# Performance work log

Hardware: AMD Instinct MI355X
Metric: run time of the kernel (lower is better)

## Reference

```python
import jax, jax.numpy as jnp
import numpy as np

H = 16  # num_heads
T, B, E = 1024, 4, 1024


def _gauss(mu, rho, eps):
    # Bayesian weight sample: sigma = log1p(exp(rho)) = softplus(rho)
    return mu + jax.nn.softplus(rho) * eps


def _rel_shift(x):
    # Transformer-XL relative shift. x: [B, H, Q, K]
    b, h, q, k = x.shape
    x = jnp.pad(x, ((0, 0), (0, 0), (0, 0), (1, 0)))  # zero col at front of K
    x = x.reshape(b, h, k + 1, q)
    return x[:, :, 1:, :].reshape(b, h, q, k)


def setup_inputs() -> dict:
    key = jax.random.key(0)
    ks = iter(jax.random.split(key, 32))
    std = float(np.sqrt(2.0 / (E + E)))

    def nrm(shape, s=std):
        return jax.random.normal(next(ks), shape, dtype=jnp.float32) * s

    def rho(shape):
        return jax.random.uniform(next(ks), shape, dtype=jnp.float32, minval=-5.0, maxval=-4.0)

    inp = {
        'x': jax.random.normal(next(ks), (T, B, E), dtype=jnp.float32),
        'pos': jax.random.normal(next(ks), (T, 1, E), dtype=jnp.float32),
        'attn_mask': jnp.triu(jnp.ones((T, T), dtype=bool), k=1),  # True = masked future
        'in_w_mu': nrm((3 * E, E)), 'in_w_rho': rho((3 * E, E)), 'in_w_eps': nrm((3 * E, E), 1.0),
        'in_b_mu': jnp.zeros((3 * E,), jnp.float32), 'in_b_rho': rho((3 * E,)), 'in_b_eps': nrm((3 * E,), 1.0),
        'pos_w_mu': nrm((E, E)), 'pos_w_rho': rho((E, E)), 'pos_w_eps': nrm((E, E), 1.0),
        'pos_b_mu': jnp.zeros((E,), jnp.float32), 'pos_b_rho': rho((E,)), 'pos_b_eps': nrm((E,), 1.0),
        'out_w_mu': nrm((E, E)), 'out_w_rho': rho((E, E)), 'out_w_eps': nrm((E, E), 1.0),
        'out_b_mu': jnp.zeros((E,), jnp.float32), 'out_b_rho': rho((E,)), 'out_b_eps': nrm((E,), 1.0),
        'rw_mu': nrm((H, E // H)), 'rw_rho': rho((H, E // H)), 'rw_eps': nrm((H, E // H), 1.0),
        'rr_mu': nrm((H, E // H)), 'rr_rho': rho((H, E // H)), 'rr_eps': nrm((H, E // H), 1.0),
    }
    return inp


def reference(x, pos, attn_mask,
              in_w_mu, in_w_rho, in_w_eps, in_b_mu, in_b_rho, in_b_eps,
              pos_w_mu, pos_w_rho, pos_w_eps, pos_b_mu, pos_b_rho, pos_b_eps,
              out_w_mu, out_w_rho, out_w_eps, out_b_mu, out_b_rho, out_b_eps,
              rw_mu, rw_rho, rw_eps, rr_mu, rr_rho, rr_eps):
    t, b, e = x.shape
    d = e // H

    in_w = _gauss(in_w_mu, in_w_rho, in_w_eps)
    in_b = _gauss(in_b_mu, in_b_rho, in_b_eps)
    pos_w = _gauss(pos_w_mu, pos_w_rho, pos_w_eps)
    pos_b = _gauss(pos_b_mu, pos_b_rho, pos_b_eps)
    out_w = _gauss(out_w_mu, out_w_rho, out_w_eps)
    out_b = _gauss(out_b_mu, out_b_rho, out_b_eps)
    r_w_bias = _gauss(rw_mu, rw_rho, rw_eps)  # [H, d]
    r_r_bias = _gauss(rr_mu, rr_rho, rr_eps)  # [H, d]

    qkv = x @ in_w.T + in_b                       # [T, B, 3E]
    q, k, v = jnp.split(qkv, 3, axis=-1)
    q = q.reshape(t, b, H, d)
    k = k.reshape(t, b, H, d)
    v = v.reshape(t, b, H, d)

    r = (pos[:, 0, :] @ pos_w.T + pos_b).reshape(-1, H, d)  # [R, H, d], R == klen

    scale = 1.0 / jnp.sqrt(jnp.asarray(d, x.dtype))
    AC = jnp.einsum('ibhd,jbhd->bhij', q + r_w_bias, k)            # content score
    BD = _rel_shift(jnp.einsum('ibhd,jhd->bhij', q + r_r_bias, r))  # position score
    scores = (AC + BD) * scale                                      # [B, H, T, T]

    neg = jnp.asarray(-1e9, scores.dtype)
    scores = jnp.where(attn_mask[None, None], neg, scores)

    probs = jax.nn.softmax(scores, axis=-1)
    ctx = jnp.einsum('bhij,jbhd->ibhd', probs, v).reshape(t, b, e)
    out = ctx @ out_w.T + out_b                   # [T, B, E]
    return out
```

## Files before the change

kernel.cpp:

```cpp
#include <hip/hip_runtime.h>

typedef unsigned short ushort_t;
typedef __attribute__((ext_vector_type(8))) short short8;
typedef __attribute__((ext_vector_type(4))) float f32x4;
typedef __attribute__((ext_vector_type(4))) unsigned short ush4;

#define MFMA_BF16(a, b, c) __builtin_amdgcn_mfma_f32_16x16x32_bf16((a), (b), (c), 0, 0, 0)

#define GLOAD_LDS16(GP, LP)                                                       \
  __builtin_amdgcn_global_load_lds(                                               \
      (const __attribute__((address_space(1))) void*)(GP),                        \
      (__attribute__((address_space(3))) void*)(LP), 16, 0, 0)

#define T_LEN 1024
#define BATCH 4
#define NHEAD 16
#define DHEAD 64
#define EMB 1024

__device__ __forceinline__ ushort_t f2bf(float f) {
  unsigned u = __float_as_uint(f);
  u += 0x7fffu + ((u >> 16) & 1u);
  return (ushort_t)(u >> 16);
}

__global__ void sample_w_kernel(const float* __restrict__ im, const float* __restrict__ ir,
                                const float* __restrict__ ie, ushort_t* __restrict__ io,
                                const float* __restrict__ pm, const float* __restrict__ pr,
                                const float* __restrict__ pe, ushort_t* __restrict__ po,
                                const float* __restrict__ om, const float* __restrict__ orh,
                                const float* __restrict__ oe, ushort_t* __restrict__ oo) {
  int i = blockIdx.x * 256 + threadIdx.x;
  const float *mu, *rho, *eps;
  ushort_t* out;
  int j;
  if (i < 786432) { mu = im; rho = ir; eps = ie; out = io; j = i; }
  else if (i < 1048576) { mu = pm; rho = pr; eps = pe; out = po; j = i - 786432; }
  else { mu = om; rho = orh; eps = oe; out = oo; j = i - 1048576; }
  f32x4 m = *(const f32x4*)(mu + (size_t)j * 4);
  f32x4 r = *(const f32x4*)(rho + (size_t)j * 4);
  f32x4 e = *(const f32x4*)(eps + (size_t)j * 4);
  ush4 o;
#pragma unroll
  for (int k = 0; k < 4; ++k) o[k] = f2bf(m[k] + log1pf(__expf(r[k])) * e[k]);
  *(ush4*)(out + (size_t)j * 4) = o;
}

__global__ void sample_bias_kernel(
    const float* __restrict__ am, const float* __restrict__ ar, const float* __restrict__ ae, float* __restrict__ ao,
    const float* __restrict__ bm, const float* __restrict__ br, const float* __restrict__ be, float* __restrict__ bo,
    const float* __restrict__ cm, const float* __restrict__ cr, const float* __restrict__ ce, float* __restrict__ co,
    const float* __restrict__ dm, const float* __restrict__ dr, const float* __restrict__ de, float* __restrict__ dof,
    const float* __restrict__ em, const float* __restrict__ er, const float* __restrict__ ee, float* __restrict__ eo) {
  int i = blockIdx.x * 256 + threadIdx.x;
  if (i < 3072) {
    ao[i] = am[i] + log1pf(__expf(ar[i])) * ae[i];
  } else if (i < 4096) {
    int j = i - 3072; bo[j] = bm[j] + log1pf(__expf(br[j])) * be[j];
  } else if (i < 5120) {
    int j = i - 4096; co[j] = cm[j] + log1pf(__expf(cr[j])) * ce[j];
  } else if (i < 6144) {
    int j = i - 5120; dof[j] = dm[j] + log1pf(__expf(dr[j])) * de[j];
  } else if (i < 7168) {
    int j = i - 6144; eo[j] = em[j] + log1pf(__expf(er[j])) * ee[j];
  }
}

__global__ void cast_bf16x4_kernel(const float* __restrict__ in, ushort_t* __restrict__ out, int n4) {
  int i = blockIdx.x * 256 + threadIdx.x;
  if (i < n4) {
    f32x4 v = *(const f32x4*)(in + (size_t)i * 4);
    ush4 o;
#pragma unroll
    for (int j = 0; j < 4; ++j) o[j] = f2bf(v[j]);
    *(ush4*)(out + (size_t)i * 4) = o;
  }
}

__global__ void zero_rhp_pad_kernel(ushort_t* __restrict__ rhp) {
  int idx = blockIdx.x * 256 + threadIdx.x;
  int dd = idx & 63;
  int pr = (idx >> 6) & 127;
  int h = idx >> 13;
  int phys = (pr < 64) ? pr : (pr - 64 + 1088);
  rhp[((size_t)h * 1152 + phys) * 64 + dd] = 0;
}

__global__ __launch_bounds__(256, 2)
void gemm_bt_kernel(const ushort_t* __restrict__ A, const ushort_t* __restrict__ Bt,
                    const float* __restrict__ bias, float* __restrict__ C,
                    int M, int N, int K) {
  __shared__ ushort_t As[128 * 32];
  __shared__ ushort_t Bs[128 * 32];
  const int tid = threadIdx.x;
  const int w = tid >> 6, l = tid & 63;
  const int m0 = blockIdx.x * 128, n0 = blockIdx.y * 128;
  const int wr = w >> 1, wc = w & 1;
  const int fr = l & 15, fk = (l >> 4) * 8;

  f32x4 acc[4][4] = {};

  for (int k0 = 0; k0 < K; k0 += 32) {
    __syncthreads();
#pragma unroll
    for (int p = 0; p < 2; ++p) {
      int c = p * 256 + tid;
      int row = c >> 2, col = (c & 3) * 8;
      GLOAD_LDS16(&A[(size_t)(m0 + row) * K + k0 + col], &As[c * 8]);
      GLOAD_LDS16(&Bt[(size_t)(n0 + row) * K + k0 + col], &Bs[c * 8]);
    }
    __syncthreads();
    short8 af[4], bf[4];
#pragma unroll
    for (int mi = 0; mi < 4; ++mi) af[mi] = *(const short8*)(&As[(wr * 64 + mi * 16 + fr) * 32 + fk]);
#pragma unroll
    for (int ni = 0; ni < 4; ++ni) bf[ni] = *(const short8*)(&Bs[(wc * 64 + ni * 16 + fr) * 32 + fk]);
#pragma unroll
    for (int mi = 0; mi < 4; ++mi)
#pragma unroll
      for (int ni = 0; ni < 4; ++ni)
        acc[mi][ni] = MFMA_BF16(af[mi], bf[ni], acc[mi][ni]);
  }

#pragma unroll
  for (int ni = 0; ni < 4; ++ni) {
    int col = n0 + wc * 64 + ni * 16 + fr;
    float bv = bias[col];
#pragma unroll
    for (int mi = 0; mi < 4; ++mi) {
#pragma unroll
      for (int q = 0; q < 4; ++q) {
        int row = m0 + wr * 64 + mi * 16 + (l >> 4) * 4 + q;
        C[(size_t)row * N + col] = acc[mi][ni][q] + bv;
      }
    }
  }
}

__global__ __launch_bounds__(256, 2)
void gemm_qkvpos_kernel(const ushort_t* __restrict__ x_bf, const ushort_t* __restrict__ in_w_bf,
                        const float* __restrict__ in_b,
                        const float* __restrict__ rwb, const float* __restrict__ rrb,
                        const ushort_t* __restrict__ posx_bf, const ushort_t* __restrict__ pos_w_bf,
                        const float* __restrict__ pos_b,
                        ushort_t* __restrict__ qrw, ushort_t* __restrict__ qrr,
                        ushort_t* __restrict__ kbuf, ushort_t* __restrict__ vt,
                        ushort_t* __restrict__ rhp) {
  __shared__ ushort_t As[128 * 32];
  __shared__ ushort_t Bs[128 * 32];
  const int K = 1024;
  const int tid = threadIdx.x;
  const int w = tid >> 6, l = tid & 63;
  const int bid = blockIdx.x;
  const bool isPos = bid >= 768;
  int m0, n0;
  const ushort_t *A, *Bt;
  if (!isPos) {
    m0 = (bid & 31) * 128; n0 = (bid >> 5) * 128; A = x_bf; Bt = in_w_bf;
  } else {
    int pb2 = bid - 768;
    m0 = (pb2 & 7) * 128; n0 = (pb2 >> 3) * 128; A = posx_bf; Bt = pos_w_bf;
  }
  const int wr = w >> 1, wc = w & 1;
  const int fr = l & 15, fk = (l >> 4) * 8;

  f32x4 acc[4][4] = {};

  for (int k0 = 0; k0 < K; k0 += 32) {
    __syncthreads();
#pragma unroll
    for (int p = 0; p < 2; ++p) {
      int c = p * 256 + tid;
      int row = c >> 2, col = (c & 3) * 8;
      GLOAD_LDS16(&A[(size_t)(m0 + row) * K + k0 + col], &As[c * 8]);
      GLOAD_LDS16(&Bt[(size_t)(n0 + row) * K + k0 + col], &Bs[c * 8]);
    }
    __syncthreads();
    short8 af[4], bf[4];
#pragma unroll
    for (int mi = 0; mi < 4; ++mi) af[mi] = *(const short8*)(&As[(wr * 64 + mi * 16 + fr) * 32 + fk]);
#pragma unroll
    for (int ni = 0; ni < 4; ++ni) bf[ni] = *(const short8*)(&Bs[(wc * 64 + ni * 16 + fr) * 32 + fk]);
#pragma unroll
    for (int mi = 0; mi < 4; ++mi)
#pragma unroll
      for (int ni = 0; ni < 4; ++ni)
        acc[mi][ni] = MFMA_BF16(af[mi], bf[ni], acc[mi][ni]);
  }

  if (!isPos) {
#pragma unroll
    for (int ni = 0; ni < 4; ++ni) {
      int col = n0 + wc * 64 + ni * 16 + fr;
      int part = col >> 10;
      int e = col & 1023;
      int hh = e >> 6, dd = e & 63;
      float bv = in_b[col];
      float rwv = rwb[e];
      float rrv = rrb[e];
#pragma unroll
      for (int mi = 0; mi < 4; ++mi) {
#pragma unroll
        for (int q = 0; q < 4; ++q) {
          int row = m0 + wr * 64 + mi * 16 + (l >> 4) * 4 + q;
          int t = row >> 2, b = row & 3;
          float v = acc[mi][ni][q] + bv;
          if (part == 0) {
            unsigned idx = (((unsigned)(b * 16 + hh) * 1024 + t) << 6) + dd;
            qrw[idx] = f2bf(v + rwv);
            qrr[idx] = f2bf(v + rrv);
          } else if (part == 1) {
            unsigned idx = (((unsigned)(b * 16 + hh) * 1024 + t) << 6) + dd;
            kbuf[idx] = f2bf(v);
          } else {
            vt[(((unsigned)(b * 16 + hh) * 64 + dd) << 10) + t] = f2bf(v);
          }
        }
      }
    }
  } else {
#pragma unroll
    for (int ni = 0; ni < 4; ++ni) {
      int col = n0 + wc * 64 + ni * 16 + fr;
      int hh = col >> 6, dd = col & 63;
      float bv = pos_b[col];
#pragma unroll
      for (int mi = 0; mi < 4; ++mi) {
#pragma unroll
        for (int q = 0; q < 4; ++q) {
          int t = m0 + wr * 64 + mi * 16 + (l >> 4) * 4 + q;
          rhp[((unsigned)hh * 1152 + 64 + t) * 64 + dd] = f2bf(acc[mi][ni][q] + bv);
        }
      }
    }
  }
}

__global__ __launch_bounds__(256, 2)
void attn_kernel(const ushort_t* __restrict__ qrw, const ushort_t* __restrict__ qrr,
                 const ushort_t* __restrict__ kb, const ushort_t* __restrict__ vt,
                 const ushort_t* __restrict__ rhp, ushort_t* __restrict__ ctx) {
  __shared__ __attribute__((aligned(16))) ushort_t KV[2][8192];
  __shared__ __attribute__((aligned(16))) char PtB[4][2048];

  const int tid = threadIdx.x, w = tid >> 6, l = tid & 63;
  const int bid = blockIdx.x;
  const int g = bid & 63;
  const int h = ((g & 7) << 1) | ((g >> 3) & 1);
  const int b = g >> 4;
  const int bh = b * 16 + h;
  const int p = bid >> 6;
  const int istA = (15 - p) * 64 + w * 16;
  const int istB = p * 64 + w * 16;
  const int njt = 16 - p;
  const int njtB = p + 1;
  const int fr = l & 15, fkq = (l >> 4) * 8;
  const float scale = 0.125f;
  char* Pw = PtB[w];

  short8 aqwA0, aqwA1, aqrA0, aqrA1, aqwB0, aqwB1, aqrB0, aqrB1;
  {
    unsigned qa = ((unsigned)bh * T_LEN + istA + fr) * 64 + fkq;
    aqwA0 = *(const short8*)(qrw + qa);
    aqwA1 = *(const short8*)(qrw + qa + 32);
    aqrA0 = *(const short8*)(qrr + qa);
    aqrA1 = *(const short8*)(qrr + qa + 32);
    unsigned qb = ((unsigned)bh * T_LEN + istB + fr) * 64 + fkq;
    aqwB0 = *(const short8*)(qrw + qb);
    aqwB1 = *(const short8*)(qrw + qb + 32);
    aqrB0 = *(const short8*)(qrr + qb);
    aqrB1 = *(const short8*)(qrr + qb + 32);
  }

  const int srow = 16 * w + (l >> 3);
  const unsigned sswz = (unsigned)(((l & 7) ^ (l >> 3)) << 4);
  const unsigned kgcol = (unsigned)(l & 7) * 8;
  const unsigned swzr = (unsigned)(fr & 7) << 4;

  const unsigned rbaseA = ((unsigned)h * 1152 + 64 + 1008 - istA + fr) * 64 + fkq;
  const unsigned rbaseB = ((unsigned)h * 1152 + 64 + 1008 - istB + fr) * 64 + fkq;

  float sA[4] = {0.f, 0.f, 0.f, 0.f}, sB[4] = {0.f, 0.f, 0.f, 0.f};
  f32x4 oA[4] = {}, oB[4] = {};

  short8 sg0, sg1, sg2, sg3;
#define STAGE_LOAD(J0)                                                              \
  do {                                                                              \
    sg0 = *(const short8*)(kb + ((unsigned)bh * 1024 + (unsigned)(J0) + srow) * 64 + kgcol);      \
    sg1 = *(const short8*)(kb + ((unsigned)bh * 1024 + (unsigned)(J0) + srow + 8) * 64 + kgcol);  \
    sg2 = *(const short8*)(vt + ((unsigned)bh * 64 + srow) * 1024 + (unsigned)(J0) + kgcol);      \
    sg3 = *(const short8*)(vt + ((unsigned)bh * 64 + srow + 8) * 1024 + (unsigned)(J0) + kgcol);  \
  } while (0)
#define STAGE_WRITE(BUF)                                                            \
  do {                                                                              \
    char* KS_ = (char*)KV[BUF];                                                     \
    *(short8*)(KS_ + (unsigned)srow * 128 + sswz) = sg0;                            \
    *(short8*)(KS_ + (unsigned)(srow + 8) * 128 + sswz) = sg1;                      \
    *(short8*)(KS_ + 8192 + (unsigned)srow * 128 + sswz) = sg2;                     \
    *(short8*)(KS_ + 8192 + (unsigned)(srow + 8) * 128 + sswz) = sg3;               \
  } while (0)

#define STRIP_TILE(AQW0, AQW1, AQR0, AQR1, RBASE, IST, SRUN, OACC)                   \
  do {                                                                               \
    short8 rf[10];                                                                   \
    unsigned roff = (RBASE) + (unsigned)j0 * 64;                                     \
    _Pragma("unroll")                                                                \
    for (int f = 0; f < 5; ++f) {                                                    \
      rf[2 * f] = *(const short8*)(rhp + roff + f * 1024);                           \
      rf[2 * f + 1] = *(const short8*)(rhp + roff + f * 1024 + 32);                  \
    }                                                                                \
    f32x4 ac[4] = {};                                                                \
    f32x4 pb[5] = {};                                                                \
    {                                                                                \
      short8 kf[8];                                                                  \
      _Pragma("unroll")                                                              \
      for (int f = 0; f < 4; ++f) {                                                  \
        unsigned rowb = (unsigned)(f * 16 + fr) * 128;                               \
        kf[2 * f] = *(const short8*)(KS + rowb + (((unsigned)fkq * 2) ^ swzr));      \
        kf[2 * f + 1] = *(const short8*)(KS + rowb + (((unsigned)fkq * 2 + 64) ^ swzr)); \
      }                                                                              \
      __builtin_amdgcn_s_setprio(1);                                                 \
      _Pragma("unroll")                                                              \
      for (int f = 0; f < 4; ++f) {                                                  \
        ac[f] = MFMA_BF16(AQW0, kf[2 * f], ac[f]);                                   \
        ac[f] = MFMA_BF16(AQW1, kf[2 * f + 1], ac[f]);                               \
      }                                                                              \
      _Pragma("unroll")                                                              \
      for (int f = 0; f < 5; ++f) {                                                  \
        pb[f] = MFMA_BF16(AQR0, rf[2 * f], pb[f]);                                   \
        pb[f] = MFMA_BF16(AQR1, rf[2 * f + 1], pb[f]);                               \
      }                                                                              \
      __builtin_amdgcn_s_setprio(0);                                                 \
    }                                                                                \
    _Pragma("unroll")                                                                \
    for (int q = 0; q < 4; ++q) {                                                    \
      int ri = 4 * (l >> 4) + q;                                                     \
      int e = 15 + fr - ri;                                                          \
      int src = (l & 48) | (e & 15);                                                 \
      float sh[5];                                                                   \
      _Pragma("unroll")                                                              \
      for (int f = 0; f < 5; ++f) sh[f] = __shfl(pb[f][q], src, 64);                 \
      int hi = e >> 4;                                                               \
      int ig = (IST) + ri;                                                           \
      _Pragma("unroll")                                                              \
      for (int ni = 0; ni < 4; ++ni) {                                               \
        float pv = hi ? sh[ni + 1] : sh[ni];                                         \
        float s = (ac[ni][q] + pv) * scale - 20.0f;                                  \
        int jg = j0 + ni * 16 + fr;                                                  \
        float pp = (jg > ig) ? 0.f : __expf(s);                                      \
        *(ushort_t*)(Pw + (((ri * 128) + (ni * 16 + fr) * 2) ^ ((ri & 7) << 4))) = f2bf(pp); \
        SRUN[q] += pp;                                                               \
      }                                                                              \
    }                                                                                \
    {                                                                                \
      short8 vf[8];                                                                  \
      _Pragma("unroll")                                                              \
      for (int dg = 0; dg < 4; ++dg) {                                               \
        unsigned rowb = 8192 + (unsigned)(dg * 16 + fr) * 128;                       \
        vf[2 * dg] = *(const short8*)(KS + rowb + (((unsigned)fkq * 2) ^ swzr));     \
        vf[2 * dg + 1] = *(const short8*)(KS + rowb + (((unsigned)(64 + fkq * 2)) ^ swzr)); \
      }                                                                              \
      short8 pa0 = *(const short8*)(Pw + ((fr * 128 + fkq * 2) ^ ((fr & 7) << 4)));  \
      short8 pa1 = *(const short8*)(Pw + ((fr * 128 + 64 + fkq * 2) ^ ((fr & 7) << 4))); \
      __builtin_amdgcn_s_setprio(1);                                                 \
      _Pragma("unroll")                                                              \
      for (int dg = 0; dg < 4; ++dg) {                                               \
        OACC[dg] = MFMA_BF16(pa0, vf[2 * dg], OACC[dg]);                             \
        OACC[dg] = MFMA_BF16(pa1, vf[2 * dg + 1], OACC[dg]);                         \
      }                                                                              \
      __builtin_amdgcn_s_setprio(0);                                                 \
    }                                                                                \
  } while (0)

  STAGE_LOAD(0);
  STAGE_WRITE(0);
  __syncthreads();

  for (int jt = 0; jt < njt; ++jt) {
    const int j0 = jt << 6;
    const char* KS = (const char*)KV[jt & 1];

    if (jt + 1 < njt) STAGE_LOAD((jt + 1) << 6);

    STRIP_TILE(aqwA0, aqwA1, aqrA0, aqrA1, rbaseA, istA, sA, oA);
    if (jt < njtB) STRIP_TILE(aqwB0, aqwB1, aqrB0, aqrB1, rbaseB, istB, sB, oB);

    if (jt + 1 < njt) STAGE_WRITE((jt + 1) & 1);
    __syncthreads();
  }

#pragma unroll
  for (int q = 0; q < 4; ++q) {
    float a = sA[q], bq = sB[q];
#pragma unroll
    for (int o2 = 8; o2; o2 >>= 1) {
      a += __shfl_xor(a, o2, 64);
      bq += __shfl_xor(bq, o2, 64);
    }
    sA[q] = a;
    sB[q] = bq;
  }
#pragma unroll
  for (int dg = 0; dg < 4; ++dg) {
#pragma unroll
    for (int q = 0; q < 4; ++q) {
      int dd = dg * 16 + fr;
      int igA = istA + 4 * (l >> 4) + q;
      ctx[((size_t)igA * BATCH + b) * EMB + h * 64 + dd] = f2bf(oA[dg][q] / sA[q]);
      int igB = istB + 4 * (l >> 4) + q;
      ctx[((size_t)igB * BATCH + b) * EMB + h * 64 + dd] = f2bf(oB[dg][q] / sB[q]);
    }
  }
}

extern "C" void kernel_launch(void* const* d_in, const int* in_sizes, int n_in,
                              void* d_out, int out_size, void* d_ws, size_t ws_size,
                              hipStream_t stream) {
  (void)in_sizes; (void)n_in; (void)out_size; (void)ws_size;
  const float* x = (const float*)d_in[0];
  const float* pos = (const float*)d_in[1];
  const float* in_w_mu = (const float*)d_in[3];
  const float* in_w_rho = (const float*)d_in[4];
  const float* in_w_eps = (const float*)d_in[5];
  const float* in_b_mu = (const float*)d_in[6];
  const float* in_b_rho = (const float*)d_in[7];
  const float* in_b_eps = (const float*)d_in[8];
  const float* pos_w_mu = (const float*)d_in[9];
  const float* pos_w_rho = (const float*)d_in[10];
  const float* pos_w_eps = (const float*)d_in[11];
  const float* pos_b_mu = (const float*)d_in[12];
  const float* pos_b_rho = (const float*)d_in[13];
  const float* pos_b_eps = (const float*)d_in[14];
  const float* out_w_mu = (const float*)d_in[15];
  const float* out_w_rho = (const float*)d_in[16];
  const float* out_w_eps = (const float*)d_in[17];
  const float* out_b_mu = (const float*)d_in[18];
  const float* out_b_rho = (const float*)d_in[19];
  const float* out_b_eps = (const float*)d_in[20];
  const float* rw_mu = (const float*)d_in[21];
  const float* rw_rho = (const float*)d_in[22];
  const float* rw_eps = (const float*)d_in[23];
  const float* rr_mu = (const float*)d_in[24];
  const float* rr_rho = (const float*)d_in[25];
  const float* rr_eps = (const float*)d_in[26];

  char* ws = (char*)d_ws;
  ushort_t* in_w_bf  = (ushort_t*)(ws + 0);
  ushort_t* pos_w_bf = (ushort_t*)(ws + 6291456);
  ushort_t* out_w_bf = (ushort_t*)(ws + 8388608);
  float* in_b  = (float*)(ws + 10485760);
  float* pos_b = (float*)(ws + 10498048);
  float* out_b = (float*)(ws + 10502144);
  float* rwb   = (float*)(ws + 10506240);
  float* rrb   = (float*)(ws + 10510336);
  ushort_t* x_bf    = (ushort_t*)(ws + 10514432);
  ushort_t* posx_bf = (ushort_t*)(ws + 18903040);
  ushort_t* qrw = (ushort_t*)(ws + 21000192);
  ushort_t* qrr = (ushort_t*)(ws + 29388800);
  ushort_t* kb  = (ushort_t*)(ws + 37777408);
  ushort_t* vt  = (ushort_t*)(ws + 46166016);
  ushort_t* rhp = (ushort_t*)(ws + 54554624);
  ushort_t* ctx = (ushort_t*)(ws + 56913920);

  sample_w_kernel<<<5120, 256, 0, stream>>>(in_w_mu, in_w_rho, in_w_eps, in_w_bf,
                                            pos_w_mu, pos_w_rho, pos_w_eps, pos_w_bf,
                                            out_w_mu, out_w_rho, out_w_eps, out_w_bf);
  sample_bias_kernel<<<28, 256, 0, stream>>>(in_b_mu, in_b_rho, in_b_eps, in_b,
                                             pos_b_mu, pos_b_rho, pos_b_eps, pos_b,
                                             out_b_mu, out_b_rho, out_b_eps, out_b,
                                             rw_mu, rw_rho, rw_eps, rwb,
                                             rr_mu, rr_rho, rr_eps, rrb);
  cast_bf16x4_kernel<<<4096, 256, 0, stream>>>(x, x_bf, 1048576);
  cast_bf16x4_kernel<<<1024, 256, 0, stream>>>(pos, posx_bf, 262144);
  zero_rhp_pad_kernel<<<512, 256, 0, stream>>>(rhp);

  gemm_qkvpos_kernel<<<832, 256, 0, stream>>>(x_bf, in_w_bf, in_b, rwb, rrb,
                                              posx_bf, pos_w_bf, pos_b,
                                              qrw, qrr, kb, vt, rhp);

  attn_kernel<<<dim3(512), 256, 0, stream>>>(qrw, qrr, kb, vt, rhp, ctx);

  gemm_bt_kernel<<<dim3(32, 8), 256, 0, stream>>>(ctx, out_w_bf, out_b, (float*)d_out, 4096, 1024, 1024);
}
```

Measured before the change: 202.4 us.

## Interleave the two query strips' score, softmax and PV stages within each tile

```diff
diff --git a/kernel.cpp b/kernel.cpp
--- a/kernel.cpp
+++ b/kernel.cpp
@@ -241,7 +241,8 @@
                  const ushort_t* __restrict__ kb, const ushort_t* __restrict__ vt,
                  const ushort_t* __restrict__ rhp, ushort_t* __restrict__ ctx) {
   __shared__ __attribute__((aligned(16))) ushort_t KV[2][8192];
-  __shared__ __attribute__((aligned(16))) char PtB[4][2048];
+  __shared__ __attribute__((aligned(16))) char PtA[4][2048];
+  __shared__ __attribute__((aligned(16))) char PtBB[4][2048];
 
   const int tid = threadIdx.x, w = tid >> 6, l = tid & 63;
   const int bid = blockIdx.x;
@@ -256,7 +257,8 @@
   const int njtB = p + 1;
   const int fr = l & 15, fkq = (l >> 4) * 8;
   const float scale = 0.125f;
-  char* Pw = PtB[w];
+  char* PwA = PtA[w];
+  char* PwB = PtBB[w];
 
   short8 aqwA0, aqwA1, aqrA0, aqrA1, aqwB0, aqwB1, aqrB0, aqrB1;
   {
@@ -300,76 +302,87 @@
     *(short8*)(KS_ + 8192 + (unsigned)(srow + 8) * 128 + sswz) = sg3;               \
   } while (0)
 
-#define STRIP_TILE(AQW0, AQW1, AQR0, AQR1, RBASE, IST, SRUN, OACC)                   \
-  do {                                                                               \
-    short8 rf[10];                                                                   \
-    unsigned roff = (RBASE) + (unsigned)j0 * 64;                                     \
-    _Pragma("unroll")                                                                \
-    for (int f = 0; f < 5; ++f) {                                                    \
-      rf[2 * f] = *(const short8*)(rhp + roff + f * 1024);                           \
-      rf[2 * f + 1] = *(const short8*)(rhp + roff + f * 1024 + 32);                  \
-    }                                                                                \
-    f32x4 ac[4] = {};                                                                \
-    f32x4 pb[5] = {};                                                                \
-    {                                                                                \
-      short8 kf[8];                                                                  \
-      _Pragma("unroll")                                                              \
-      for (int f = 0; f < 4; ++f) {                                                  \
-        unsigned rowb = (unsigned)(f * 16 + fr) * 128;                               \
-        kf[2 * f] = *(const short8*)(KS + rowb + (((unsigned)fkq * 2) ^ swzr));      \
-        kf[2 * f + 1] = *(const short8*)(KS + rowb + (((unsigned)fkq * 2 + 64) ^ swzr)); \
-      }                                                                              \
-      __builtin_amdgcn_s_setprio(1);                                                 \
-      _Pragma("unroll")                                                              \
-      for (int f = 0; f < 4; ++f) {                                                  \
-        ac[f] = MFMA_BF16(AQW0, kf[2 * f], ac[f]);                                   \
-        ac[f] = MFMA_BF16(AQW1, kf[2 * f + 1], ac[f]);                               \
-      }                                                                              \
-      _Pragma("unroll")                                                              \
-      for (int f = 0; f < 5; ++f) {                                                  \
-        pb[f] = MFMA_BF16(AQR0, rf[2 * f], pb[f]);                                   \
-        pb[f] = MFMA_BF16(AQR1, rf[2 * f + 1], pb[f]);                               \
-      }                                                                              \
-      __builtin_amdgcn_s_setprio(0);                                                 \
-    }                                                                                \
-    _Pragma("unroll")                                                                \
-    for (int q = 0; q < 4; ++q) {                                                    \
-      int ri = 4 * (l >> 4) + q;                                                     \
-      int e = 15 + fr - ri;                                                          \
-      int src = (l & 48) | (e & 15);                                                 \
-      float sh[5];                                                                   \
-      _Pragma("unroll")                                                              \
-      for (int f = 0; f < 5; ++f) sh[f] = __shfl(pb[f][q], src, 64);                 \
-      int hi = e >> 4;                                                               \
-      int ig = (IST) + ri;                                                           \
-      _Pragma("unroll")                                                              \
-      for (int ni = 0; ni < 4; ++ni) {                                               \
-        float pv = hi ? sh[ni + 1] : sh[ni];                                         \
-        float s = (ac[ni][q] + pv) * scale - 20.0f;                                  \
-        int jg = j0 + ni * 16 + fr;                                                  \
-        float pp = (jg > ig) ? 0.f : __expf(s);                                      \
-        *(ushort_t*)(Pw + (((ri * 128) + (ni * 16 + fr) * 2) ^ ((ri & 7) << 4))) = f2bf(pp); \
-        SRUN[q] += pp;                                                               \
-      }                                                                              \
-    }                                                                                \
-    {                                                                                \
-      short8 vf[8];                                                                  \
-      _Pragma("unroll")                                                              \
-      for (int dg = 0; dg < 4; ++dg) {                                               \
-        unsigned rowb = 8192 + (unsigned)(dg * 16 + fr) * 128;                       \
-        vf[2 * dg] = *(const short8*)(KS + rowb + (((unsigned)fkq * 2) ^ swzr));     \
-        vf[2 * dg + 1] = *(const short8*)(KS + rowb + (((unsigned)(64 + fkq * 2)) ^ swzr)); \
-      }                                                                              \
-      short8 pa0 = *(const short8*)(Pw + ((fr * 128 + fkq * 2) ^ ((fr & 7) << 4)));  \
-      short8 pa1 = *(const short8*)(Pw + ((fr * 128 + 64 + fkq * 2) ^ ((fr & 7) << 4))); \
-      __builtin_amdgcn_s_setprio(1);                                                 \
-      _Pragma("unroll")                                                              \
-      for (int dg = 0; dg < 4; ++dg) {                                               \
-        OACC[dg] = MFMA_BF16(pa0, vf[2 * dg], OACC[dg]);                             \
-        OACC[dg] = MFMA_BF16(pa1, vf[2 * dg + 1], OACC[dg]);                         \
-      }                                                                              \
-      __builtin_amdgcn_s_setprio(0);                                                 \
-    }                                                                                \
+#define RF_LOAD(RF, RBASE)                                                          \
+  do {                                                                              \
+    unsigned roff = (RBASE) + (unsigned)j0 * 64;                                    \
+    _Pragma("unroll")                                                               \
+    for (int f = 0; f < 5; ++f) {                                                   \
+      RF[2 * f] = *(const short8*)(rhp + roff + f * 1024);                          \
+      RF[2 * f + 1] = *(const short8*)(rhp + roff + f * 1024 + 32);                 \
+    }                                                                               \
+  } while (0)
+
+#define KF_LOAD(KF)                                                                 \
+  do {                                                                              \
+    _Pragma("unroll")                                                               \
+    for (int f = 0; f < 4; ++f) {                                                   \
+      unsigned rowb = (unsigned)(f * 16 + fr) * 128;                                \
+      KF[2 * f] = *(const short8*)(KS + rowb + (((unsigned)fkq * 2) ^ swzr));       \
+      KF[2 * f + 1] = *(const short8*)(KS + rowb + (((unsigned)fkq * 2 + 64) ^ swzr)); \
+    }                                                                               \
+  } while (0)
+
+#define VF_LOAD(VF)                                                                 \
+  do {                                                                              \
+    _Pragma("unroll")                                                               \
+    for (int dg = 0; dg < 4; ++dg) {                                                \
+      unsigned rowb = 8192 + (unsigned)(dg * 16 + fr) * 128;                        \
+      VF[2 * dg] = *(const short8*)(KS + rowb + (((unsigned)fkq * 2) ^ swzr));      \
+      VF[2 * dg + 1] = *(const short8*)(KS + rowb + (((unsigned)(64 + fkq * 2)) ^ swzr)); \
+    }                                                                               \
+  } while (0)
+
+#define SCORE(AC, PB, KF, RF, AQW0, AQW1, AQR0, AQR1)                               \
+  do {                                                                              \
+    __builtin_amdgcn_s_setprio(1);                                                  \
+    _Pragma("unroll")                                                               \
+    for (int f = 0; f < 4; ++f) {                                                   \
+      AC[f] = MFMA_BF16(AQW0, KF[2 * f], AC[f]);                                    \
+      AC[f] = MFMA_BF16(AQW1, KF[2 * f + 1], AC[f]);                                \
+    }                                                                               \
+    _Pragma("unroll")                                                               \
+    for (int f = 0; f < 5; ++f) {                                                   \
+      PB[f] = MFMA_BF16(AQR0, RF[2 * f], PB[f]);                                    \
+      PB[f] = MFMA_BF16(AQR1, RF[2 * f + 1], PB[f]);                                \
+    }                                                                               \
+    __builtin_amdgcn_s_setprio(0);                                                  \
+  } while (0)
+
+#define GATHER(AC, PB, IST, SRUN, PW)                                               \
+  do {                                                                              \
+    _Pragma("unroll")                                                               \
+    for (int q = 0; q < 4; ++q) {                                                   \
+      int ri = 4 * (l >> 4) + q;                                                    \
+      int e = 15 + fr - ri;                                                         \
+      int src = (l & 48) | (e & 15);                                                \
+      float sh[5];                                                                  \
+      _Pragma("unroll")                                                             \
+      for (int f = 0; f < 5; ++f) sh[f] = __shfl(PB[f][q], src, 64);                \
+      int hi = e >> 4;                                                              \
+      int ig = (IST) + ri;                                                          \
+      _Pragma("unroll")                                                             \
+      for (int ni = 0; ni < 4; ++ni) {                                              \
+        float pv = hi ? sh[ni + 1] : sh[ni];                                        \
+        float s = (AC[ni][q] + pv) * scale - 20.0f;                                 \
+        int jg = j0 + ni * 16 + fr;                                                 \
+        float pp = (jg > ig) ? 0.f : __expf(s);                                     \
+        *(ushort_t*)((PW) + (((ri * 128) + (ni * 16 + fr) * 2) ^ ((ri & 7) << 4))) = f2bf(pp); \
+        SRUN[q] += pp;                                                              \
+      }                                                                             \
+    }                                                                               \
+  } while (0)
+
+#define PVACC(OACC, PW, VF)                                                         \
+  do {                                                                              \
+    short8 pa0 = *(const short8*)((PW) + ((fr * 128 + fkq * 2) ^ ((fr & 7) << 4))); \
+    short8 pa1 = *(const short8*)((PW) + ((fr * 128 + 64 + fkq * 2) ^ ((fr & 7) << 4))); \
+    __builtin_amdgcn_s_setprio(1);                                                  \
+    _Pragma("unroll")                                                               \
+    for (int dg = 0; dg < 4; ++dg) {                                                \
+      OACC[dg] = MFMA_BF16(pa0, VF[2 * dg], OACC[dg]);                              \
+      OACC[dg] = MFMA_BF16(pa1, VF[2 * dg + 1], OACC[dg]);                          \
+    }                                                                               \
+    __builtin_amdgcn_s_setprio(0);                                                  \
   } while (0)
 
   STAGE_LOAD(0);
@@ -382,8 +395,40 @@
 
     if (jt + 1 < njt) STAGE_LOAD((jt + 1) << 6);
 
-    STRIP_TILE(aqwA0, aqwA1, aqrA0, aqrA1, rbaseA, istA, sA, oA);
-    if (jt < njtB) STRIP_TILE(aqwB0, aqwB1, aqrB0, aqrB1, rbaseB, istB, sB, oB);
+    if (jt < njtB) {
+      short8 rfA[10];
+      RF_LOAD(rfA, rbaseA);
+      short8 kfA[8];
+      KF_LOAD(kfA);
+      f32x4 acA[4] = {};
+      f32x4 pbA[5] = {};
+      SCORE(acA, pbA, kfA, rfA, aqwA0, aqwA1, aqrA0, aqrA1);
+      short8 rfB[10];
+      RF_LOAD(rfB, rbaseB);
+      short8 vf[8];
+      VF_LOAD(vf);
+      GATHER(acA, pbA, istA, sA, PwA);
+      short8 kfB[8];
+      KF_LOAD(kfB);
+      f32x4 acB[4] = {};
+      f32x4 pbB[5] = {};
+      SCORE(acB, pbB, kfB, rfB, aqwB0, aqwB1, aqrB0, aqrB1);
+      GATHER(acB, pbB, istB, sB, PwB);
+      PVACC(oA, PwA, vf);
+      PVACC(oB, PwB, vf);
+    } else {
+      short8 rfA[10];
+      RF_LOAD(rfA, rbaseA);
+      short8 kfA[8];
+      KF_LOAD(kfA);
+      f32x4 acA[4] = {};
+      f32x4 pbA[5] = {};
+      SCORE(acA, pbA, kfA, rfA, aqwA0, aqwA1, aqrA0, aqrA1);
+      short8 vf[8];
+      VF_LOAD(vf);
+      GATHER(acA, pbA, istA, sA, PwA);
+      PVACC(oA, PwA, vf);
+    }
 
     if (jt + 1 < njt) STAGE_WRITE((jt + 1) & 1);
     __syncthreads();
```

Result: slower. 363.9 us (+79.8%).
